# Optimization experiments

Measured on AMD Instinct MI355X. Metric: run time of the kernel, lower is better.

The kernel has to match this reference:

```python
import jax, jax.numpy as jnp
import numpy as np

N, HID, NH = 4096, 1024, 8
D = HID // NH            # ret_size = 128
F_SCALE = 1.0
GAMMA = 1.0 - 2.0 ** (-5)
SCALE_EXP = D ** (-0.5)
LN_EPS = 1e-5


def setup_inputs() -> dict:
    key = jax.random.key(0)
    ks = jax.random.split(key, 12)
    s = HID ** (-0.5)
    return {
        "cur_hiddens": jax.random.normal(ks[0], (N, HID), jnp.float32),
        "f_adj": jax.random.uniform(ks[1], (N, N), jnp.float32),
        "f_dist": jax.random.uniform(ks[2], (N, N), jnp.float32),
        "f_clb": jax.random.normal(ks[3], (N, N), jnp.float32),
        "Wq": jax.random.normal(ks[4], (HID, HID), jnp.float32) * s,
        "Wk": jax.random.normal(ks[5], (HID, HID), jnp.float32) * s,
        "Wv": jax.random.normal(ks[6], (HID, HID), jnp.float32) * s,
        "Wo": jax.random.normal(ks[7], (HID, HID), jnp.float32) * s,
        "bo": jax.random.normal(ks[8], (HID,), jnp.float32) * 0.01,
        "ln_g": jnp.ones((HID,), jnp.float32),
        "ln_b": jnp.zeros((HID,), jnp.float32),
    }


def _layer_norm(x, g, b):
    mu = jnp.mean(x, axis=-1, keepdims=True)
    var = jnp.mean(jnp.square(x - mu), axis=-1, keepdims=True)
    return (x - mu) * jax.lax.rsqrt(var + LN_EPS) * g + b


def reference(cur_hiddens, f_adj, f_dist, f_clb, Wq, Wk, Wv, Wo, bo, ln_g, ln_b):
    n = cur_hiddens.shape[0]
    # projections, reshaped to (heads, atoms, ret_size)
    q = (cur_hiddens @ Wq).reshape(n, NH, D).transpose(1, 0, 2)
    k = (cur_hiddens @ Wk).reshape(n, NH, D).transpose(1, 0, 2)
    v = (cur_hiddens @ Wv).reshape(n, NH, D).transpose(1, 0, 2)
    # retention scores per head: (NH, n, n)
    scores = jnp.einsum('hnd,hmd->hnm', q, k)
    # per-head structural bias injection (no softmax on scores)
    adj_b = F_SCALE * f_adj
    dist_b = F_SCALE * jax.nn.softmax(f_dist, axis=1)
    clb_b = F_SCALE * jax.nn.softmax(f_clb, axis=1)
    scores = scores.at[0].add(adj_b).at[1].add(adj_b)
    scores = scores.at[2].add(dist_b).at[3].add(dist_b)
    scores = scores.at[4].add(clb_b).at[5].add(clb_b)
    scores = scores * (GAMMA ** SCALE_EXP)
    # retention output
    ret = jnp.einsum('hnm,hmd->hnd', scores, v)
    ret = jax.nn.relu(ret)                          # act_func (dropout p=0)
    ret = ret.transpose(1, 0, 2).reshape(n, HID)    # (n, NH*D)
    out = ret @ Wo + bo
    mol_vec = _layer_norm(cur_hiddens + out, ln_g, ln_b)
    return mol_vec, jnp.mean(scores, axis=0)
```

## Files before the change

### kernel.cpp

```cpp
#include <hip/hip_runtime.h>
#include <math.h>

#define NA     4096
#define HID    1024
#define LN_EPS 1e-5f

typedef short s8   __attribute__((ext_vector_type(8)));
typedef float f32x4 __attribute__((ext_vector_type(4)));

#define OFF_XBF   ((size_t)0)
#define OFF_WQT   ((size_t)8<<20)
#define OFF_WKT   ((size_t)10<<20)
#define OFF_WVT   ((size_t)12<<20)
#define OFF_QB    ((size_t)14<<20)
#define OFF_KB    ((size_t)22<<20)
#define OFF_VB    ((size_t)30<<20)
#define OFF_RETB  OFF_VB
#define OFF_KT    ((size_t)38<<20)
#define OFF_VT    ((size_t)46<<20)
#define OFF_WOT   ((size_t)54<<20)
#define OFF_M2F   ((size_t)56<<20)
#define OFF_M2B   (OFF_M2F + ((size_t)512<<10))
#define OFF_RMAXD (OFF_M2F + ((size_t)768<<10))
#define OFF_RINVD (OFF_RMAXD + 16384)
#define OFF_RMAXC (OFF_RINVD + 16384)
#define OFF_RINVC (OFF_RMAXC + 16384)
#define OFF_YF    ((size_t)0)

__device__ __forceinline__ ushort f2bf(float f) {
    unsigned u = __float_as_uint(f);
    u += 0x7FFFu + ((u >> 16) & 1u);
    return (ushort)(u >> 16);
}

__device__ __forceinline__ void mfma_step(const short* As, const short* Bs,
                                          f32x4 (&acc)[4][4], int lane, int wr, int wc)
{
    const int r = lane & 15, kg = (lane >> 4) * 8;
    s8 a[4], b[4];
#pragma unroll
    for (int i = 0; i < 4; i++) a[i] = *(const s8*)&As[(wr*64 + i*16 + r)*32 + kg];
#pragma unroll
    for (int j = 0; j < 4; j++) b[j] = *(const s8*)&Bs[(wc*64 + j*16 + r)*32 + kg];
#pragma unroll
    for (int i = 0; i < 4; i++)
#pragma unroll
        for (int j = 0; j < 4; j++)
            acc[i][j] = __builtin_amdgcn_mfma_f32_16x16x32_bf16(a[i], b[j], acc[i][j], 0, 0, 0);
}

__device__ __forceinline__ void gemm_bf16_nt(const ushort* A, int lda,
    const ushort* Bt, int ldb, int K, int row0, int col0,
    short* As, short* Bs, f32x4 (&acc)[4][4], int tid)
{
    const int lane = tid & 63, wave = tid >> 6, wr = wave >> 1, wc = wave & 1;
    const int sr = tid >> 1, sc = (tid & 1) * 16;
    const ushort* Ap = A  + (size_t)(row0 + sr) * lda + sc;
    const ushort* Bp = Bt + (size_t)(col0 + sr) * ldb + sc;
    short* Ad = &As[sr * 32 + sc];
    short* Bd = &Bs[sr * 32 + sc];
    for (int kt = 0; kt < K; kt += 32) {
        uint4 a0 = *(const uint4*)(Ap + kt);
        uint4 a1 = *(const uint4*)(Ap + kt + 8);
        uint4 b0 = *(const uint4*)(Bp + kt);
        uint4 b1 = *(const uint4*)(Bp + kt + 8);
        __syncthreads();
        *(uint4*)Ad = a0; *(uint4*)(Ad + 8) = a1;
        *(uint4*)Bd = b0; *(uint4*)(Bd + 8) = b1;
        __syncthreads();
        mfma_step(As, Bs, acc, lane, wr, wc);
    }
}

#define ZERO_ACC(acc) { f32x4 z = {0.f,0.f,0.f,0.f}; \
    _Pragma("unroll") for (int i=0;i<4;i++) _Pragma("unroll") for (int j=0;j<4;j++) acc[i][j]=z; }

__global__ __launch_bounds__(256) void k_prep(const float* __restrict__ X,
    const float* __restrict__ Wq, const float* __restrict__ Wk,
    const float* __restrict__ Wv, const float* __restrict__ Wo, char* __restrict__ wsb)
{
    const int z = blockIdx.z, bx = blockIdx.x, by = blockIdx.y, t = threadIdx.x;
    const int lr = t >> 2, jb = t & 3;
    if (z == 0) {
        const float* src = X + (size_t)(by*64 + lr) * HID + bx*64 + jb*16;
        ushort* dst = (ushort*)(wsb + OFF_XBF) + (size_t)(by*64 + lr) * HID + bx*64 + jb*16;
        union { ushort u[16]; uint4 q[2]; } pk;
        union { float f[16]; float4 v[4]; } fa;
#pragma unroll
        for (int m = 0; m < 4; m++) fa.v[m] = ((const float4*)src)[m];
#pragma unroll
        for (int m = 0; m < 16; m++) pk.u[m] = f2bf(fa.f[m]);
        ((uint4*)dst)[0] = pk.q[0]; ((uint4*)dst)[1] = pk.q[1];
        return;
    }
    if (by >= 16) return;
    __shared__ ushort Tl[64][72];
    const float* W = (z == 1) ? Wq : (z == 2) ? Wk : (z == 3) ? Wv : Wo;
    ushort* WT = (ushort*)(wsb + ((z==1)?OFF_WQT:(z==2)?OFF_WKT:(z==3)?OFF_WVT:OFF_WOT));
    const int r0 = by*64, c0 = bx*64;
    const float* src = W + (size_t)(r0 + lr) * HID + c0 + jb*16;
    union { float f[16]; float4 v[4]; } fa;
#pragma unroll
    for (int m = 0; m < 4; m++) fa.v[m] = ((const float4*)src)[m];
#pragma unroll
    for (int m = 0; m < 16; m++) Tl[lr][jb*16 + m] = f2bf(fa.f[m]);
    __syncthreads();
    union { ushort u[16]; uint4 q[2]; } pk;
#pragma unroll
    for (int m = 0; m < 16; m++) pk.u[m] = Tl[jb*16 + m][lr];
    ushort* dst = WT + (size_t)(c0 + lr) * HID + r0 + jb*16;
    ((uint4*)dst)[0] = pk.q[0]; ((uint4*)dst)[1] = pk.q[1];
}

__global__ __launch_bounds__(256) void k_rowstats(const float* __restrict__ f_dist,
    const float* __restrict__ f_clb, char* __restrict__ wsb)
{
    const int row = blockIdx.x, mat = blockIdx.y, t = threadIdx.x;
    const float* F = mat ? f_clb : f_dist;
    float* rmax = (float*)(wsb + (mat ? OFF_RMAXC : OFF_RMAXD));
    float* rinv = (float*)(wsb + (mat ? OFF_RINVC : OFF_RINVD));
    float4 v[4];
#pragma unroll
    for (int p = 0; p < 4; p++)
        v[p] = *(const float4*)(F + (size_t)row * NA + 4*t + 1024*p);
    float m = -1e30f;
#pragma unroll
    for (int p = 0; p < 4; p++)
        m = fmaxf(m, fmaxf(fmaxf(v[p].x, v[p].y), fmaxf(v[p].z, v[p].w)));
    for (int off = 32; off; off >>= 1) m = fmaxf(m, __shfl_xor(m, off));
    __shared__ float sb[4];
    if ((t & 63) == 0) sb[t >> 6] = m;
    __syncthreads();
    const float m4 = fmaxf(fmaxf(sb[0], sb[1]), fmaxf(sb[2], sb[3]));
    __syncthreads();
    float s = 0.f;
#pragma unroll
    for (int p = 0; p < 4; p++)
        s += expf(v[p].x-m4) + expf(v[p].y-m4) + expf(v[p].z-m4) + expf(v[p].w-m4);
    for (int off = 32; off; off >>= 1) s += __shfl_xor(s, off);
    if ((t & 63) == 0) sb[t >> 6] = s;
    __syncthreads();
    if (t == 0) { rmax[row] = m4; rinv[row] = 1.0f / (sb[0]+sb[1]+sb[2]+sb[3]); }
}

__global__ __launch_bounds__(256) void k_proj(char* __restrict__ wsb)
{
    __shared__ __align__(16) short As[4096], Bs[4096];
    const int z = blockIdx.z;
    const ushort* A  = (const ushort*)(wsb + OFF_XBF);
    const ushort* Bt = (const ushort*)(wsb + ((z==0)?OFF_WQT:(z==1)?OFF_WKT:OFF_WVT));
    ushort* O = (ushort*)(wsb + ((z==0)?OFF_QB:(z==1)?OFF_KB:OFF_VB));
    const int row0 = blockIdx.y*128, col0 = blockIdx.x*128;
    f32x4 acc[4][4]; ZERO_ACC(acc);
    gemm_bf16_nt(A, HID, Bt, HID, HID, row0, col0, As, Bs, acc, threadIdx.x);
    const int lane = threadIdx.x & 63, wave = threadIdx.x >> 6, wr = wave>>1, wc = wave&1;
#pragma unroll
    for (int i = 0; i < 4; i++)
#pragma unroll
    for (int e = 0; e < 4; e++) {
        const int r = row0 + wr*64 + i*16 + (lane>>4)*4 + e;
#pragma unroll
        for (int j = 0; j < 4; j++) {
            const int c = col0 + wc*64 + j*16 + (lane & 15);
            O[(size_t)r*HID + c] = f2bf(acc[i][j][e]);
        }
    }
}

__global__ __launch_bounds__(256) void k_transKV(char* __restrict__ wsb)
{
    const int z = blockIdx.z;
    const ushort* in = (const ushort*)(wsb + (z ? OFF_VB : OFF_KB));
    ushort* out = (ushort*)(wsb + (z ? OFF_VT : OFF_KT));
    const int n0 = blockIdx.y*64, c0 = blockIdx.x*64;
    const int t = threadIdx.x, lr = t >> 2, jb = t & 3;
    __shared__ ushort Tl[64][72];
    const ushort* src = in + (size_t)(n0 + lr) * HID + c0 + jb*16;
    union { ushort u[16]; uint4 q[2]; } pk;
    pk.q[0] = ((const uint4*)src)[0]; pk.q[1] = ((const uint4*)src)[1];
#pragma unroll
    for (int m = 0; m < 16; m++) Tl[lr][jb*16 + m] = pk.u[m];
    __syncthreads();
#pragma unroll
    for (int m = 0; m < 16; m++) pk.u[m] = Tl[jb*16 + m][lr];
    ushort* dst = out + (size_t)(c0 + lr) * NA + n0 + jb*16;
    ((uint4*)dst)[0] = pk.q[0]; ((uint4*)dst)[1] = pk.q[1];
}

__global__ __launch_bounds__(256) void k_ktv(char* __restrict__ wsb)
{
    __shared__ __align__(16) short As[4096], Bs[4096];
    const int ci = blockIdx.x, h = blockIdx.y;
    const ushort* A  = (const ushort*)(wsb + OFF_VT) + (size_t)h*128*NA + ci*256;
    const ushort* Bt = (const ushort*)(wsb + OFF_KT) + (size_t)h*128*NA + ci*256;
    f32x4 acc[4][4]; ZERO_ACC(acc);
    gemm_bf16_nt(A, NA, Bt, NA, 256, 0, 0, As, Bs, acc, threadIdx.x);
    float* M2f = (float*)(wsb + OFF_M2F) + (size_t)h*16384;
    const int lane = threadIdx.x & 63, wave = threadIdx.x >> 6, wr = wave>>1, wc = wave&1;
#pragma unroll
    for (int i = 0; i < 4; i++)
#pragma unroll
    for (int e = 0; e < 4; e++) {
        const int r = wr*64 + i*16 + (lane>>4)*4 + e;
#pragma unroll
        for (int j = 0; j < 4; j++) {
            const int c = wc*64 + j*16 + (lane & 15);
            atomicAdd(&M2f[r*128 + c], acc[i][j][e]);
        }
    }
}

__global__ __launch_bounds__(256) void k_m2cvt(char* __restrict__ wsb)
{
    const int i = (blockIdx.x*256 + threadIdx.x) * 8;
    const float* s = (const float*)(wsb + OFF_M2F);
    ushort* d = (ushort*)(wsb + OFF_M2B);
    union { float f[8]; float4 v[2]; } fa;
    fa.v[0] = *(const float4*)(s + i); fa.v[1] = *(const float4*)(s + i + 4);
    union { ushort u[8]; uint4 q; } pk;
#pragma unroll
    for (int m = 0; m < 8; m++) pk.u[m] = f2bf(fa.f[m]);
    *(uint4*)(d + i) = pk.q;
}

__global__ __launch_bounds__(256) void k_scores(char* __restrict__ wsb,
    const float* __restrict__ f_adj, const float* __restrict__ f_dist,
    const float* __restrict__ f_clb, float* __restrict__ outs, float cdiv8, float cdiv4)
{
    __shared__ __align__(16) short As[4096], Bs[4096];
    const int row0 = blockIdx.y*128, col0 = blockIdx.x*128;
    f32x4 acc[4][4]; ZERO_ACC(acc);
    gemm_bf16_nt((const ushort*)(wsb + OFF_QB), HID,
                 (const ushort*)(wsb + OFF_KB), HID, HID, row0, col0, As, Bs, acc, threadIdx.x);
    const float* rmaxd = (const float*)(wsb + OFF_RMAXD);
    const float* rinvd = (const float*)(wsb + OFF_RINVD);
    const float* rmaxc = (const float*)(wsb + OFF_RMAXC);
    const float* rinvc = (const float*)(wsb + OFF_RINVC);
    const int lane = threadIdx.x & 63, wave = threadIdx.x >> 6, wr = wave>>1, wc = wave&1;
#pragma unroll
    for (int i = 0; i < 4; i++)
#pragma unroll
    for (int e = 0; e < 4; e++) {
        const int r = row0 + wr*64 + i*16 + (lane>>4)*4 + e;
        const float rmd = rmaxd[r], rid = rinvd[r], rmc = rmaxc[r], ric = rinvc[r];
#pragma unroll
        for (int j = 0; j < 4; j++) {
            const int c = col0 + wc*64 + j*16 + (lane & 15);
            const size_t idx = (size_t)r * NA + c;
            const float bias = f_adj[idx] + __expf(f_dist[idx]-rmd)*rid
                                          + __expf(f_clb[idx]-rmc)*ric;
            outs[idx] = cdiv8 * acc[i][j][e] + cdiv4 * bias;
        }
    }
}

__global__ __launch_bounds__(256) void k_ret(char* __restrict__ wsb,
    const float* __restrict__ f_adj, const float* __restrict__ f_dist,
    const float* __restrict__ f_clb, float c_scale)
{
    __shared__ __align__(16) short As[4096], Bs[4096];
    const int p = blockIdx.z, x = blockIdx.x, row0 = blockIdx.y*128;
    const int tid = threadIdx.x, lane = tid & 63, wave = tid >> 6, wr = wave>>1, wc = wave&1;
    const int sr = tid >> 1, sc = (tid & 1) * 16;
    const int h = (p < 3) ? p*2 + x : 6 + x;
    f32x4 acc[4][4]; ZERO_ACC(acc);
    short* Ad = &As[sr*32 + sc];
    short* Bd = &Bs[sr*32 + sc];

    if (p < 3) {
        const float* F = (p == 0) ? f_adj : (p == 1) ? f_dist : f_clb;
        const bool sm = (p > 0);
        float rm = 0.f, ri = 1.f;
        if (sm) {
            const float* RM = (const float*)(wsb + ((p==1) ? OFF_RMAXD : OFF_RMAXC));
            const float* RI = (const float*)(wsb + ((p==1) ? OFF_RINVD : OFF_RINVC));
            rm = RM[row0 + sr]; ri = RI[row0 + sr];
        }
        const float* Fp = F + (size_t)(row0 + sr) * NA + sc;
        const ushort* Bp = (const ushort*)(wsb + OFF_VT) + (size_t)(p*256 + x*128 + sr) * NA + sc;
        for (int kt = 0; kt < NA; kt += 32) {
            union { float f[16]; float4 v[4]; } fa;
#pragma unroll
            for (int m = 0; m < 4; m++) fa.v[m] = *(const float4*)(Fp + kt + m*4);
            uint4 b0 = *(const uint4*)(Bp + kt);
            uint4 b1 = *(const uint4*)(Bp + kt + 8);
            if (sm) {
#pragma unroll
                for (int m = 0; m < 16; m++) fa.f[m] = __expf(fa.f[m] - rm) * ri;
            }
            union { ushort u[16]; uint4 q[2]; } pk;
#pragma unroll
            for (int m = 0; m < 16; m++) pk.u[m] = f2bf(fa.f[m]);
            __syncthreads();
            *(uint4*)Ad = pk.q[0]; *(uint4*)(Ad + 8) = pk.q[1];
            *(uint4*)Bd = b0;      *(uint4*)(Bd + 8) = b1;
            __syncthreads();
            mfma_step(As, Bs, acc, lane, wr, wc);
        }
    }
    const ushort* Ap2 = (const ushort*)(wsb + OFF_QB) + (size_t)(row0 + sr) * HID + h*128 + sc;
    const ushort* Bp2 = (const ushort*)(wsb + OFF_M2B) + (size_t)h*16384 + sr*128 + sc;
    for (int kt = 0; kt < 128; kt += 32) {
        uint4 a0 = *(const uint4*)(Ap2 + kt), a1 = *(const uint4*)(Ap2 + kt + 8);
        uint4 b0 = *(const uint4*)(Bp2 + kt), b1 = *(const uint4*)(Bp2 + kt + 8);
        __syncthreads();
        *(uint4*)Ad = a0; *(uint4*)(Ad + 8) = a1;
        *(uint4*)Bd = b0; *(uint4*)(Bd + 8) = b1;
        __syncthreads();
        mfma_step(As, Bs, acc, lane, wr, wc);
    }
    ushort* R = (ushort*)(wsb + OFF_RETB);
#pragma unroll
    for (int i = 0; i < 4; i++)
#pragma unroll
    for (int e = 0; e < 4; e++) {
        const int r = row0 + wr*64 + i*16 + (lane>>4)*4 + e;
#pragma unroll
        for (int j = 0; j < 4; j++) {
            const int c = wc*64 + j*16 + (lane & 15);
            R[(size_t)r*HID + h*128 + c] = f2bf(fmaxf(c_scale * acc[i][j][e], 0.f));
        }
    }
}

__global__ __launch_bounds__(256) void k_wo(char* __restrict__ wsb,
    const float* __restrict__ X, const float* __restrict__ bo)
{
    __shared__ __align__(16) short As[4096], Bs[4096];
    const int row0 = blockIdx.y*128, col0 = blockIdx.x*128;
    f32x4 acc[4][4]; ZERO_ACC(acc);
    gemm_bf16_nt((const ushort*)(wsb + OFF_RETB), HID,
                 (const ushort*)(wsb + OFF_WOT), HID, HID, row0, col0, As, Bs, acc, threadIdx.x);
    float* Y = (float*)(wsb + OFF_YF);
    const int lane = threadIdx.x & 63, wave = threadIdx.x >> 6, wr = wave>>1, wc = wave&1;
#pragma unroll
    for (int i = 0; i < 4; i++)
#pragma unroll
    for (int e = 0; e < 4; e++) {
        const int r = row0 + wr*64 + i*16 + (lane>>4)*4 + e;
#pragma unroll
        for (int j = 0; j < 4; j++) {
            const int c = col0 + wc*64 + j*16 + (lane & 15);
            Y[(size_t)r*HID + c] = acc[i][j][e] + X[(size_t)r*HID + c] + bo[c];
        }
    }
}

__global__ __launch_bounds__(256) void k_ln(const char* __restrict__ wsb,
    const float* __restrict__ g, const float* __restrict__ b, float* __restrict__ out)
{
    const float* Y = (const float*)(wsb + OFF_YF);
    const int row = blockIdx.x, t = threadIdx.x;
    float4 v = *(const float4*)(Y + (size_t)row * HID + 4*t);
    float s = v.x + v.y + v.z + v.w;
    for (int off = 32; off; off >>= 1) s += __shfl_xor(s, off);
    __shared__ float sb[4];
    if ((t & 63) == 0) sb[t >> 6] = s;
    __syncthreads();
    const float mu = (sb[0]+sb[1]+sb[2]+sb[3]) * (1.0f / HID);
    const float dx = v.x-mu, dy = v.y-mu, dz = v.z-mu, dw = v.w-mu;
    float q = dx*dx + dy*dy + dz*dz + dw*dw;
    __syncthreads();
    for (int off = 32; off; off >>= 1) q += __shfl_xor(q, off);
    if ((t & 63) == 0) sb[t >> 6] = q;
    __syncthreads();
    const float var = (sb[0]+sb[1]+sb[2]+sb[3]) * (1.0f / HID);
    const float rstd = rsqrtf(var + LN_EPS);
    float4 gv = *(const float4*)(g + 4*t);
    float4 bv = *(const float4*)(b + 4*t);
    float4 o = make_float4(dx*rstd*gv.x + bv.x, dy*rstd*gv.y + bv.y,
                           dz*rstd*gv.z + bv.z, dw*rstd*gv.w + bv.w);
    *(float4*)(out + (size_t)row * HID + 4*t) = o;
}

extern "C" void kernel_launch(void* const* d_in, const int* in_sizes, int n_in,
                              void* d_out, int out_size, void* d_ws, size_t ws_size,
                              hipStream_t stream)
{
    const float* X      = (const float*)d_in[0];
    const float* f_adj  = (const float*)d_in[1];
    const float* f_dist = (const float*)d_in[2];
    const float* f_clb  = (const float*)d_in[3];
    const float* Wq     = (const float*)d_in[4];
    const float* Wk     = (const float*)d_in[5];
    const float* Wv     = (const float*)d_in[6];
    const float* Wo     = (const float*)d_in[7];
    const float* bo     = (const float*)d_in[8];
    const float* ln_g   = (const float*)d_in[9];
    const float* ln_b   = (const float*)d_in[10];

    char* wsb = (char*)d_ws;
    float* out = (float*)d_out;
    float* out_scores = out + (size_t)NA * HID;

    const float c_scale = (float)pow(1.0 - 1.0/32.0, 1.0 / sqrt(128.0));

    hipMemsetAsync(wsb + OFF_M2F, 0, (size_t)512 << 10, stream);

    k_prep    <<<dim3(16, 64, 5), 256, 0, stream>>>(X, Wq, Wk, Wv, Wo, wsb);
    k_rowstats<<<dim3(NA, 2),     256, 0, stream>>>(f_dist, f_clb, wsb);
    k_proj    <<<dim3(8, 32, 3),  256, 0, stream>>>(wsb);
    k_transKV <<<dim3(16, 64, 2), 256, 0, stream>>>(wsb);
    k_ktv     <<<dim3(16, 8),     256, 0, stream>>>(wsb);
    k_m2cvt   <<<64,              256, 0, stream>>>(wsb);
    k_scores  <<<dim3(32, 32),    256, 0, stream>>>(wsb, f_adj, f_dist, f_clb,
                                                    out_scores, c_scale/8.f, c_scale/4.f);
    k_ret     <<<dim3(2, 32, 4),  256, 0, stream>>>(wsb, f_adj, f_dist, f_clb, c_scale);
    k_wo      <<<dim3(8, 32),     256, 0, stream>>>(wsb, X, bo);
    k_ln      <<<NA,              256, 0, stream>>>(wsb, ln_g, ln_b, out);
}
```

Baseline: 613.8 us.

## Split-K retention GEMM with atomic fp32 partials, wider tiles, padded LDS rows

Padding the LDS row stride from 32 to 40 shorts is meant to cut bank conflicts in every MFMA GEMM. The bias-times-V retention kernel is rewritten to split K into four chunks. Each 512-thread block now covers both heads sharing a bias matrix with a 128x256 tile, so each f_* element is loaded and exponentiated once instead of twice. Partial results are atomically added into an fp32 buffer, and a separate finishing kernel adds the Q·M2 term, scale and ReLU. This trades more blocks and less duplicated bias traffic for a 12 MB memset, fp32 atomics, and an extra kernel launch.

```diff
diff --git a/kernel.cpp b/kernel.cpp
--- a/kernel.cpp
+++ b/kernel.cpp
@@ -4,6 +4,7 @@
 #define NA     4096
 #define HID    1024
 #define LN_EPS 1e-5f
+#define LDSW   40
 
 typedef short s8   __attribute__((ext_vector_type(8)));
 typedef float f32x4 __attribute__((ext_vector_type(4)));
@@ -15,7 +16,6 @@
 #define OFF_QB    ((size_t)14<<20)
 #define OFF_KB    ((size_t)22<<20)
 #define OFF_VB    ((size_t)30<<20)
-#define OFF_RETB  OFF_VB
 #define OFF_KT    ((size_t)38<<20)
 #define OFF_VT    ((size_t)46<<20)
 #define OFF_WOT   ((size_t)54<<20)
@@ -25,6 +25,8 @@
 #define OFF_RINVD (OFF_RMAXD + 16384)
 #define OFF_RMAXC (OFF_RINVD + 16384)
 #define OFF_RINVC (OFF_RMAXC + 16384)
+#define OFF_RETF  ((size_t)22<<20)
+#define OFF_RETB  ((size_t)34<<20)
 #define OFF_YF    ((size_t)0)
 
 __device__ __forceinline__ ushort f2bf(float f) {
@@ -33,15 +35,15 @@
     return (ushort)(u >> 16);
 }
 
-__device__ __forceinline__ void mfma_step(const short* As, const short* Bs,
+__device__ __forceinline__ void mfma_tile(const short* As, const short* Bs,
                                           f32x4 (&acc)[4][4], int lane, int wr, int wc)
 {
     const int r = lane & 15, kg = (lane >> 4) * 8;
     s8 a[4], b[4];
 #pragma unroll
-    for (int i = 0; i < 4; i++) a[i] = *(const s8*)&As[(wr*64 + i*16 + r)*32 + kg];
-#pragma unroll
-    for (int j = 0; j < 4; j++) b[j] = *(const s8*)&Bs[(wc*64 + j*16 + r)*32 + kg];
+    for (int i = 0; i < 4; i++) a[i] = *(const s8*)&As[(wr*64 + i*16 + r)*LDSW + kg];
+#pragma unroll
+    for (int j = 0; j < 4; j++) b[j] = *(const s8*)&Bs[(wc*64 + j*16 + r)*LDSW + kg];
 #pragma unroll
     for (int i = 0; i < 4; i++)
 #pragma unroll
@@ -57,8 +59,8 @@
     const int sr = tid >> 1, sc = (tid & 1) * 16;
     const ushort* Ap = A  + (size_t)(row0 + sr) * lda + sc;
     const ushort* Bp = Bt + (size_t)(col0 + sr) * ldb + sc;
-    short* Ad = &As[sr * 32 + sc];
-    short* Bd = &Bs[sr * 32 + sc];
+    short* Ad = &As[sr * LDSW + sc];
+    short* Bd = &Bs[sr * LDSW + sc];
     for (int kt = 0; kt < K; kt += 32) {
         uint4 a0 = *(const uint4*)(Ap + kt);
         uint4 a1 = *(const uint4*)(Ap + kt + 8);
@@ -68,7 +70,7 @@
         *(uint4*)Ad = a0; *(uint4*)(Ad + 8) = a1;
         *(uint4*)Bd = b0; *(uint4*)(Bd + 8) = b1;
         __syncthreads();
-        mfma_step(As, Bs, acc, lane, wr, wc);
+        mfma_tile(As, Bs, acc, lane, wr, wc);
     }
 }
 
@@ -145,7 +147,7 @@
 
 __global__ __launch_bounds__(256) void k_proj(char* __restrict__ wsb)
 {
-    __shared__ __align__(16) short As[4096], Bs[4096];
+    __shared__ __align__(16) short As[128*LDSW], Bs[128*LDSW];
     const int z = blockIdx.z;
     const ushort* A  = (const ushort*)(wsb + OFF_XBF);
     const ushort* Bt = (const ushort*)(wsb + ((z==0)?OFF_WQT:(z==1)?OFF_WKT:OFF_WVT));
@@ -189,7 +191,7 @@
 
 __global__ __launch_bounds__(256) void k_ktv(char* __restrict__ wsb)
 {
-    __shared__ __align__(16) short As[4096], Bs[4096];
+    __shared__ __align__(16) short As[128*LDSW], Bs[128*LDSW];
     const int ci = blockIdx.x, h = blockIdx.y;
     const ushort* A  = (const ushort*)(wsb + OFF_VT) + (size_t)h*128*NA + ci*256;
     const ushort* Bt = (const ushort*)(wsb + OFF_KT) + (size_t)h*128*NA + ci*256;
@@ -227,7 +229,7 @@
     const float* __restrict__ f_adj, const float* __restrict__ f_dist,
     const float* __restrict__ f_clb, float* __restrict__ outs, float cdiv8, float cdiv4)
 {
-    __shared__ __align__(16) short As[4096], Bs[4096];
+    __shared__ __align__(16) short As[128*LDSW], Bs[128*LDSW];
     const int row0 = blockIdx.y*128, col0 = blockIdx.x*128;
     f32x4 acc[4][4]; ZERO_ACC(acc);
     gemm_bf16_nt((const ushort*)(wsb + OFF_QB), HID,
@@ -254,62 +256,52 @@
     }
 }
 
-__global__ __launch_bounds__(256) void k_ret(char* __restrict__ wsb,
+__global__ __launch_bounds__(512, 2) void k_ret2(char* __restrict__ wsb,
     const float* __restrict__ f_adj, const float* __restrict__ f_dist,
-    const float* __restrict__ f_clb, float c_scale)
-{
-    __shared__ __align__(16) short As[4096], Bs[4096];
-    const int p = blockIdx.z, x = blockIdx.x, row0 = blockIdx.y*128;
-    const int tid = threadIdx.x, lane = tid & 63, wave = tid >> 6, wr = wave>>1, wc = wave&1;
-    const int sr = tid >> 1, sc = (tid & 1) * 16;
-    const int h = (p < 3) ? p*2 + x : 6 + x;
-    f32x4 acc[4][4]; ZERO_ACC(acc);
-    short* Ad = &As[sr*32 + sc];
-    short* Bd = &Bs[sr*32 + sc];
-
-    if (p < 3) {
-        const float* F = (p == 0) ? f_adj : (p == 1) ? f_dist : f_clb;
-        const bool sm = (p > 0);
-        float rm = 0.f, ri = 1.f;
-        if (sm) {
-            const float* RM = (const float*)(wsb + ((p==1) ? OFF_RMAXD : OFF_RMAXC));
-            const float* RI = (const float*)(wsb + ((p==1) ? OFF_RINVD : OFF_RINVC));
-            rm = RM[row0 + sr]; ri = RI[row0 + sr];
-        }
-        const float* Fp = F + (size_t)(row0 + sr) * NA + sc;
-        const ushort* Bp = (const ushort*)(wsb + OFF_VT) + (size_t)(p*256 + x*128 + sr) * NA + sc;
-        for (int kt = 0; kt < NA; kt += 32) {
-            union { float f[16]; float4 v[4]; } fa;
-#pragma unroll
-            for (int m = 0; m < 4; m++) fa.v[m] = *(const float4*)(Fp + kt + m*4);
-            uint4 b0 = *(const uint4*)(Bp + kt);
-            uint4 b1 = *(const uint4*)(Bp + kt + 8);
-            if (sm) {
-#pragma unroll
-                for (int m = 0; m < 16; m++) fa.f[m] = __expf(fa.f[m] - rm) * ri;
-            }
-            union { ushort u[16]; uint4 q[2]; } pk;
-#pragma unroll
-            for (int m = 0; m < 16; m++) pk.u[m] = f2bf(fa.f[m]);
-            __syncthreads();
-            *(uint4*)Ad = pk.q[0]; *(uint4*)(Ad + 8) = pk.q[1];
-            *(uint4*)Bd = b0;      *(uint4*)(Bd + 8) = b1;
-            __syncthreads();
-            mfma_step(As, Bs, acc, lane, wr, wc);
-        }
-    }
-    const ushort* Ap2 = (const ushort*)(wsb + OFF_QB) + (size_t)(row0 + sr) * HID + h*128 + sc;
-    const ushort* Bp2 = (const ushort*)(wsb + OFF_M2B) + (size_t)h*16384 + sr*128 + sc;
-    for (int kt = 0; kt < 128; kt += 32) {
-        uint4 a0 = *(const uint4*)(Ap2 + kt), a1 = *(const uint4*)(Ap2 + kt + 8);
-        uint4 b0 = *(const uint4*)(Bp2 + kt), b1 = *(const uint4*)(Bp2 + kt + 8);
+    const float* __restrict__ f_clb)
+{
+    __shared__ __align__(16) short As[128*LDSW];
+    __shared__ __align__(16) short Bs[256*LDSW];
+    const int kc = blockIdx.x;
+    const int row0 = blockIdx.y * 128;
+    const int p = blockIdx.z;
+    const int tid = threadIdx.x, lane = tid & 63, wave = tid >> 6;
+    const int wr = wave >> 2, wc = wave & 3;
+    const int ar = tid >> 2, ac = (tid & 3) * 8;
+    const int br = tid >> 1, bc = (tid & 1) * 16;
+
+    const float* F = (p == 0) ? f_adj : (p == 1) ? f_dist : f_clb;
+    float rm = 0.f, ri = 1.f;
+    if (p) {
+        rm = ((const float*)(wsb + ((p==1) ? OFF_RMAXD : OFF_RMAXC)))[row0 + ar];
+        ri = ((const float*)(wsb + ((p==1) ? OFF_RINVD : OFF_RINVC)))[row0 + ar];
+    }
+    const float*  Fp = F + (size_t)(row0 + ar) * NA + kc*1024 + ac;
+    const ushort* Bp = (const ushort*)(wsb + OFF_VT) + (size_t)(p*256 + br) * NA + kc*1024 + bc;
+    short* Ad = &As[ar * LDSW + ac];
+    short* Bd = &Bs[br * LDSW + bc];
+
+    f32x4 acc[4][4]; ZERO_ACC(acc);
+    for (int kt = 0; kt < 1024; kt += 32) {
+        union { float f[8]; float4 v[2]; } fa;
+        fa.v[0] = *(const float4*)(Fp + kt);
+        fa.v[1] = *(const float4*)(Fp + kt + 4);
+        uint4 b0 = *(const uint4*)(Bp + kt);
+        uint4 b1 = *(const uint4*)(Bp + kt + 8);
+        if (p) {
+#pragma unroll
+            for (int m = 0; m < 8; m++) fa.f[m] = __expf(fa.f[m] - rm) * ri;
+        }
+        union { ushort u[8]; uint4 q; } pk;
+#pragma unroll
+        for (int m = 0; m < 8; m++) pk.u[m] = f2bf(fa.f[m]);
         __syncthreads();
-        *(uint4*)Ad = a0; *(uint4*)(Ad + 8) = a1;
+        *(uint4*)Ad = pk.q;
         *(uint4*)Bd = b0; *(uint4*)(Bd + 8) = b1;
         __syncthreads();
-        mfma_step(As, Bs, acc, lane, wr, wc);
-    }
-    ushort* R = (ushort*)(wsb + OFF_RETB);
+        mfma_tile(As, Bs, acc, lane, wr, wc);
+    }
+    float* RF = (float*)(wsb + OFF_RETF);
 #pragma unroll
     for (int i = 0; i < 4; i++)
 #pragma unroll
@@ -317,8 +309,35 @@
         const int r = row0 + wr*64 + i*16 + (lane>>4)*4 + e;
 #pragma unroll
         for (int j = 0; j < 4; j++) {
-            const int c = wc*64 + j*16 + (lane & 15);
-            R[(size_t)r*HID + h*128 + c] = f2bf(fmaxf(c_scale * acc[i][j][e], 0.f));
+            const int c = p*256 + wc*64 + j*16 + (lane & 15);
+            atomicAdd(&RF[(size_t)r * 768 + c], acc[i][j][e]);
+        }
+    }
+}
+
+__global__ __launch_bounds__(256) void k_retfin(char* __restrict__ wsb, float c_scale)
+{
+    __shared__ __align__(16) short As[128*LDSW], Bs[128*LDSW];
+    const int h = blockIdx.x, row0 = blockIdx.y * 128;
+    const ushort* A  = (const ushort*)(wsb + OFF_QB) + (size_t)row0 * HID + h*128;
+    const ushort* Bt = (const ushort*)(wsb + OFF_M2B) + (size_t)h * 16384;
+    f32x4 acc[4][4]; ZERO_ACC(acc);
+    gemm_bf16_nt(A, HID, Bt, 128, 128, 0, 0, As, Bs, acc, threadIdx.x);
+    const float* RF = (const float*)(wsb + OFF_RETF);
+    ushort* RB = (ushort*)(wsb + OFF_RETB);
+    const int lane = threadIdx.x & 63, wave = threadIdx.x >> 6, wr = wave>>1, wc = wave&1;
+#pragma unroll
+    for (int i = 0; i < 4; i++)
+#pragma unroll
+    for (int e = 0; e < 4; e++) {
+        const int r = row0 + wr*64 + i*16 + (lane>>4)*4 + e;
+#pragma unroll
+        for (int j = 0; j < 4; j++) {
+            const int cl = wc*64 + j*16 + (lane & 15);
+            const int col = h*128 + cl;
+            float v = acc[i][j][e];
+            if (h < 6) v += RF[(size_t)r * 768 + col];
+            RB[(size_t)r * HID + col] = f2bf(fmaxf(c_scale * v, 0.f));
         }
     }
 }
@@ -326,7 +345,7 @@
 __global__ __launch_bounds__(256) void k_wo(char* __restrict__ wsb,
     const float* __restrict__ X, const float* __restrict__ bo)
 {
-    __shared__ __align__(16) short As[4096], Bs[4096];
+    __shared__ __align__(16) short As[128*LDSW], Bs[128*LDSW];
     const int row0 = blockIdx.y*128, col0 = blockIdx.x*128;
     f32x4 acc[4][4]; ZERO_ACC(acc);
     gemm_bf16_nt((const ushort*)(wsb + OFF_RETB), HID,
@@ -405,7 +424,9 @@
     k_m2cvt   <<<64,              256, 0, stream>>>(wsb);
     k_scores  <<<dim3(32, 32),    256, 0, stream>>>(wsb, f_adj, f_dist, f_clb,
                                                     out_scores, c_scale/8.f, c_scale/4.f);
-    k_ret     <<<dim3(2, 32, 4),  256, 0, stream>>>(wsb, f_adj, f_dist, f_clb, c_scale);
+    hipMemsetAsync(wsb + OFF_RETF, 0, (size_t)NA * 768 * 4, stream);
+    k_ret2    <<<dim3(4, 32, 3),  512, 0, stream>>>(wsb, f_adj, f_dist, f_clb);
+    k_retfin  <<<dim3(8, 32),     256, 0, stream>>>(wsb, c_scale);
     k_wo      <<<dim3(8, 32),     256, 0, stream>>>(wsb, X, bo);
     k_ln      <<<NA,              256, 0, stream>>>(wsb, ln_g, ln_b, out);
 }
```

New measurement: 551.6 us. 1.11x faster.
